# Performance work log

Measured on AMD Instinct MI355X. Metric: run time of the kernel, lower is better.

Reference implementation:

```python
import jax, jax.numpy as jnp
import numpy as np

N, D, B = 131072, 256, 16

def setup_inputs() -> dict:
    key = jax.random.key(0)
    k1, k2, k3 = jax.random.split(key, 3)
    inp = jax.random.normal(k1, (N, D), dtype=jnp.float32)
    tgt = jax.random.normal(k2, (N, D), dtype=jnp.float32)
    batch = jnp.sort(jax.random.randint(k3, (N,), 0, B, dtype=jnp.int64))
    return {"input": inp, "target": tgt, "batch": batch, "batch_size": B}

def reference(input, target, batch, batch_size):
    # Per-node squared errors for sign +1 and sign -1.  [N]
    sq_pos = jnp.sum((input - target) ** 2, axis=-1)
    sq_neg = jnp.sum((-input - target) ** 2, axis=-1)
    # Per-graph losses via segment sum.  [B]
    loss_pos = jax.ops.segment_sum(sq_pos, batch, num_segments=batch_size)
    loss_neg = jax.ops.segment_sum(sq_neg, batch, num_segments=batch_size)
    # Global brute-force argmin over 2^B sign vectors decomposes per graph;
    # ties go to +1 (all-(+1) is the first combination in itertools.product).
    signs = jnp.where(loss_pos <= loss_neg, 1.0, -1.0).astype(input.dtype)
    signs = jax.lax.stop_gradient(signs)  # torch builds signs from detached tensors
    signed_input = input * signs[batch][:, None]
    # F.mse_loss(..., reduction='sum')
    return jnp.sum((signed_input - target) ** 2)
```

## Files before the change

kernel.cpp:

```cpp
#include <hip/hip_runtime.h>

#define N_ROWS 131072
#define D_COLS 256
#define B_SEG  16
#define ROWS_PER_WAVE 16
#define NSLOT 64

__global__ __launch_bounds__(256) void umse_main(
    const float* __restrict__ input,
    const float* __restrict__ target,
    const int*   __restrict__ batch,
    float*       __restrict__ acc ) {

    const int wave = (blockIdx.x * blockDim.x + threadIdx.x) >> 6;
    const int lane = threadIdx.x & 63;
    const int row0 = wave * ROWS_PER_WAVE;
    float* __restrict__ slot = acc + (blockIdx.x & (NSLOT - 1)) * (B_SEG * 2);

    const float4* __restrict__ in4 = (const float4*)input;
    const float4* __restrict__ tg4 = (const float4*)target;

    const int b0 = batch[row0];
    const int b1 = batch[row0 + ROWS_PER_WAVE - 1];

    if (b0 == b1) {
        float rp0 = 0.f, rn0 = 0.f, rp1 = 0.f, rn1 = 0.f;
        float rp2 = 0.f, rn2 = 0.f, rp3 = 0.f, rn3 = 0.f;
        #pragma unroll
        for (int half = 0; half < 2; ++half) {
            const int base = (row0 + half * 8) * (D_COLS / 4) + lane;
            float4 xa[8], ta[8];
            #pragma unroll
            for (int i = 0; i < 8; ++i) xa[i] = in4[base + i * (D_COLS / 4)];
            #pragma unroll
            for (int i = 0; i < 8; ++i) ta[i] = tg4[base + i * (D_COLS / 4)];
            #pragma unroll
            for (int i = 0; i < 8; ++i) {
                float d;
                d = xa[i].x - ta[i].x; rp0 += d * d;  d = xa[i].x + ta[i].x; rn0 += d * d;
                d = xa[i].y - ta[i].y; rp1 += d * d;  d = xa[i].y + ta[i].y; rn1 += d * d;
                d = xa[i].z - ta[i].z; rp2 += d * d;  d = xa[i].z + ta[i].z; rn2 += d * d;
                d = xa[i].w - ta[i].w; rp3 += d * d;  d = xa[i].w + ta[i].w; rn3 += d * d;
            }
        }
        float rp = (rp0 + rp1) + (rp2 + rp3);
        float rn = (rn0 + rn1) + (rn2 + rn3);
        #pragma unroll
        for (int off = 32; off; off >>= 1) {
            rp += __shfl_down(rp, off);
            rn += __shfl_down(rn, off);
        }
        if (lane == 0) {
            atomicAdd(&slot[b0 * 2 + 0], rp);
            atomicAdd(&slot[b0 * 2 + 1], rn);
        }
    } else {
        for (int i = 0; i < ROWS_PER_WAVE; ++i) {
            const int r = row0 + i;
            const int b = batch[r];
            const float4 x = in4[r * (D_COLS / 4) + lane];
            const float4 t = tg4[r * (D_COLS / 4) + lane];
            float d;
            float p = 0.f, n = 0.f;
            d = x.x - t.x; p += d * d;  d = x.x + t.x; n += d * d;
            d = x.y - t.y; p += d * d;  d = x.y + t.y; n += d * d;
            d = x.z - t.z; p += d * d;  d = x.z + t.z; n += d * d;
            d = x.w - t.w; p += d * d;  d = x.w + t.w; n += d * d;
            #pragma unroll
            for (int off = 32; off; off >>= 1) {
                p += __shfl_down(p, off);
                n += __shfl_down(n, off);
            }
            if (lane == 0) {
                atomicAdd(&slot[b * 2 + 0], p);
                atomicAdd(&slot[b * 2 + 1], n);
            }
        }
    }
}

__global__ void umse_final(const float* __restrict__ acc, float* __restrict__ out) {
    const int lane = threadIdx.x;
    float s = 0.f;
    if (lane < B_SEG * 2) {
        #pragma unroll
        for (int sl = 0; sl < NSLOT; ++sl)
            s += acc[sl * (B_SEG * 2) + lane];
    }
    const float partner = __shfl_xor(s, 1);
    const float m = fminf(s, partner);
    float contrib = ((lane < B_SEG * 2) && ((lane & 1) == 0)) ? m : 0.f;
    #pragma unroll
    for (int off = 32; off; off >>= 1)
        contrib += __shfl_down(contrib, off);
    if (lane == 0) out[0] = contrib;
}

extern "C" void kernel_launch(void* const* d_in, const int* in_sizes, int n_in,
                              void* d_out, int out_size, void* d_ws, size_t ws_size,
                              hipStream_t stream) {
    const float* input  = (const float*)d_in[0];
    const float* target = (const float*)d_in[1];
    const int*   batch  = (const int*)d_in[2];
    float* acc = (float*)d_ws;

    hipMemsetAsync(acc, 0, NSLOT * B_SEG * 2 * sizeof(float), stream);

    const int waves  = N_ROWS / ROWS_PER_WAVE;
    const int blocks = waves * 64 / 256;
    umse_main<<<blocks, 256, 0, stream>>>(input, target, batch, acc);
    umse_final<<<1, 64, 0, stream>>>(acc, (float*)d_out);
}
```

Baseline: 55.53 us.

## Replace per-wave atomics with per-wave partial writes and overflow records

Each uniform wave now writes its two partial sums to its own slot instead of doing atomicAdd into a shared slot array, so contended global atomics are gone from the hot path. Waves that span a segment boundary build local per-segment sums and append one record to an overflow buffer through a counter. The final kernel grows to 1024 threads, scans all 8192 wave partials plus the overflow records, and resets the counter. This trades atomic contention for a heavier single-block reduction kernel.

```diff
diff --git a/kernel.cpp b/kernel.cpp
--- a/kernel.cpp
+++ b/kernel.cpp
@@ -4,18 +4,20 @@
 #define D_COLS 256
 #define B_SEG  16
 #define ROWS_PER_WAVE 16
-#define NSLOT 64
+#define NWAVE (N_ROWS / ROWS_PER_WAVE)
+
 
 __global__ __launch_bounds__(256) void umse_main(
     const float* __restrict__ input,
     const float* __restrict__ target,
     const int*   __restrict__ batch,
-    float*       __restrict__ acc ) {
+    float*       __restrict__ part ,
+    int*         __restrict__ ovtk ,
+    float*       __restrict__ ovfl ) {
 
     const int wave = (blockIdx.x * blockDim.x + threadIdx.x) >> 6;
     const int lane = threadIdx.x & 63;
     const int row0 = wave * ROWS_PER_WAVE;
-    float* __restrict__ slot = acc + (blockIdx.x & (NSLOT - 1)) * (B_SEG * 2);
 
     const float4* __restrict__ in4 = (const float4*)input;
     const float4* __restrict__ tg4 = (const float4*)target;
@@ -51,10 +53,13 @@
             rn += __shfl_down(rn, off);
         }
         if (lane == 0) {
-            atomicAdd(&slot[b0 * 2 + 0], rp);
-            atomicAdd(&slot[b0 * 2 + 1], rn);
+            float2* p = (float2*)&part[wave * 2];
+            *p = make_float2(rp, rn);
         }
     } else {
+        float lp[B_SEG], ln[B_SEG];
+        #pragma unroll
+        for (int k = 0; k < B_SEG; ++k) { lp[k] = 0.f; ln[k] = 0.f; }
         for (int i = 0; i < ROWS_PER_WAVE; ++i) {
             const int r = row0 + i;
             const int b = batch[r];
@@ -72,28 +77,83 @@
                 n += __shfl_down(n, off);
             }
             if (lane == 0) {
-                atomicAdd(&slot[b * 2 + 0], p);
-                atomicAdd(&slot[b * 2 + 1], n);
+                const int k = b - b0;
+                #pragma unroll
+                for (int kk = 0; kk < B_SEG; ++kk) {
+                    if (kk == k) { lp[kk] += p; ln[kk] += n; }
+                }
             }
+        }
+        if (lane == 0) {
+            part[wave * 2 + 0] = 0.f;
+            part[wave * 2 + 1] = 0.f;
+            const int slot = atomicAdd(ovtk, 1);
+            float* line = &ovfl[slot * 33];
+            #pragma unroll
+            for (int k = 0; k < B_SEG; ++k) {
+                line[2 * k + 0] = lp[k];
+                line[2 * k + 1] = ln[k];
+            }
+            line[32] = (float)b0;
         }
     }
 }
 
-__global__ void umse_final(const float* __restrict__ acc, float* __restrict__ out) {
-    const int lane = threadIdx.x;
-    float s = 0.f;
-    if (lane < B_SEG * 2) {
+__global__ __launch_bounds__(1024) void umse_final(
+    const float* __restrict__ part,
+    const int*   __restrict__ batch,
+    int*         __restrict__ ovtk,
+    const float* __restrict__ ovfl,
+    float*       __restrict__ out) {
+
+    __shared__ float gacc[B_SEG * 2];
+    const int tid = threadIdx.x;
+    if (tid < B_SEG * 2) gacc[tid] = 0.f;
+    __syncthreads();
+
+    float lp = 0.f, ln = 0.f;
+    int cur = -1;
+    for (int w = tid; w < NWAVE; w += 1024) {
+        const int b = batch[w * ROWS_PER_WAVE];
+        if (b != cur) {
+            if (cur >= 0) {
+                atomicAdd(&gacc[cur * 2 + 0], lp);
+                atomicAdd(&gacc[cur * 2 + 1], ln);
+            }
+            cur = b; lp = 0.f; ln = 0.f;
+        }
+        lp += part[w * 2 + 0];
+        ln += part[w * 2 + 1];
+    }
+    if (cur >= 0) {
+        atomicAdd(&gacc[cur * 2 + 0], lp);
+        atomicAdd(&gacc[cur * 2 + 1], ln);
+    }
+    __syncthreads();
+
+    if (tid == 0) {
+        const int nov = *ovtk;
+        float acc2[B_SEG * 2];
         #pragma unroll
-        for (int sl = 0; sl < NSLOT; ++sl)
-            s += acc[sl * (B_SEG * 2) + lane];
+        for (int k = 0; k < B_SEG * 2; ++k) acc2[k] = gacc[k];
+        for (int s = 0; s < nov; ++s) {
+            const float* line = &ovfl[s * 33];
+            const int base = (int)line[32];
+            for (int k = 0; k < B_SEG; ++k) {
+                const int b = base + k;
+                if (b < B_SEG) {
+                    acc2[b * 2 + 0] += line[2 * k + 0];
+                    acc2[b * 2 + 1] += line[2 * k + 1];
+                }
+            }
+        }
+        float s = 0.f;
+        #pragma unroll
+        for (int b = 0; b < B_SEG; ++b)
+            s += fminf(acc2[2 * b + 0], acc2[2 * b + 1]);
+        out[0] = s;
+        *ovtk = 0;
     }
-    const float partner = __shfl_xor(s, 1);
-    const float m = fminf(s, partner);
-    float contrib = ((lane < B_SEG * 2) && ((lane & 1) == 0)) ? m : 0.f;
-    #pragma unroll
-    for (int off = 32; off; off >>= 1)
-        contrib += __shfl_down(contrib, off);
-    if (lane == 0) out[0] = contrib;
 }
 
 extern "C" void kernel_launch(void* const* d_in, const int* in_sizes, int n_in,
@@ -102,12 +162,14 @@
     const float* input  = (const float*)d_in[0];
     const float* target = (const float*)d_in[1];
     const int*   batch  = (const int*)d_in[2];
-    float* acc = (float*)d_ws;
 
-    hipMemsetAsync(acc, 0, NSLOT * B_SEG * 2 * sizeof(float), stream);
+    float* part = (float*)d_ws;
+    int*   ovtk = (int*)((char*)d_ws + NWAVE * 2 * sizeof(float));
+    float* ovfl = (float*)((char*)ovtk + 256);
 
-    const int waves  = N_ROWS / ROWS_PER_WAVE;
-    const int blocks = waves * 64 / 256;
-    umse_main<<<blocks, 256, 0, stream>>>(input, target, batch, acc);
-    umse_final<<<1, 64, 0, stream>>>(acc, (float*)d_out);
+    hipMemsetAsync(ovtk, 0, sizeof(int), stream);
+
+    const int blocks = NWAVE * 64 / 256;
+    umse_main<<<blocks, 256, 0, stream>>>(input, target, batch, part, ovtk, ovfl);
+    umse_final<<<1, 1024, 0, stream>>>(part, batch, ovtk, ovfl, (float*)d_out);
 }
```

Result: slower. 96.57 us (+73.9%).
